# Performance work log

Hardware: AMD Instinct MI355X
Metric: run time of the kernel (lower is better)

The kernel has to match this reference:

```python
import jax, jax.numpy as jnp
import numpy as np

# Level-7 icosphere: nv vertices, nf faces
NV, NF = 163842, 327680
IN_C, NECK_C, OUT_C, B = 64, 32, 128, 2
EPS = 1e-5


def setup_inputs() -> dict:
    key = jax.random.key(0)
    ks = jax.random.split(key, 16)
    f32 = jnp.float32
    d = {}
    d['x'] = jax.random.normal(ks[0], (B, IN_C, NV), f32)
    # conv1 (1x1), bn1
    d['w1'] = jax.random.normal(ks[1], (NECK_C, IN_C), f32) * 0.05
    d['b1'] = jnp.zeros((NECK_C,), f32)
    d['gamma1'] = jnp.ones((NECK_C,), f32); d['beta1'] = jnp.zeros((NECK_C,), f32)
    # MeshConv: coeffs (out,in,4 taps: id, lap, grad_ew, grad_ns) + bias
    d['coeffs'] = jax.random.normal(ks[2], (NECK_C, NECK_C, 4), f32) * 0.05
    d['mc_bias'] = jnp.zeros((NECK_C,), f32)
    d['gamma2'] = jnp.ones((NECK_C,), f32); d['beta2'] = jnp.zeros((NECK_C,), f32)
    # conv3 (1x1), bn3
    d['w3'] = jax.random.normal(ks[3], (OUT_C, NECK_C), f32) * 0.05
    d['b3'] = jnp.zeros((OUT_C,), f32)
    d['gamma3'] = jnp.ones((OUT_C,), f32); d['beta3'] = jnp.zeros((OUT_C,), f32)
    # shortcut conv_ + bn_ (diff_chan since in!=out)
    d['wsc'] = jax.random.normal(ks[4], (OUT_C, IN_C), f32) * 0.05
    d['bsc'] = jnp.zeros((OUT_C,), f32)
    d['gammasc'] = jnp.ones((OUT_C,), f32); d['betasc'] = jnp.zeros((OUT_C,), f32)
    # sparse mesh operators (gather indices + values):
    # G: face gradient, 3 components per face from 3 face vertices
    d['idx_G'] = jax.random.randint(ks[5], (NF, 3), 0, NV, jnp.int32)
    d['vals_G'] = jax.random.normal(ks[6], (NF, 3, 3), f32) * 0.1
    # EW/NS tangent direction per face (3-vectors)
    d['EW'] = jax.random.normal(ks[7], (NF, 3), f32)
    d['NS'] = jax.random.normal(ks[8], (NF, 3), f32)
    # L: vertex laplacian, ~7 nnz per row
    d['idx_L'] = jax.random.randint(ks[9], (NV, 7), 0, NV, jnp.int32)
    d['vals_L'] = jax.random.normal(ks[10], (NV, 7), f32) * 0.1
    # F2V: face-to-vertex averaging, ~6 faces per vertex
    d['idx_F2V'] = jax.random.randint(ks[11], (NV, 6), 0, NF, jnp.int32)
    d['vals_F2V'] = jax.random.uniform(ks[12], (NV, 6), f32) / 6.0
    return d


def _bn(x, g, b):
    # training-mode BatchNorm1d over (batch, spatial), per channel
    m = x.mean(axis=(0, 2), keepdims=True)
    v = ((x - m) ** 2).mean(axis=(0, 2), keepdims=True)
    return g[None, :, None] * (x - m) * jax.lax.rsqrt(v + EPS) + b[None, :, None]


def _conv1x1(x, w, b):
    return jnp.einsum('oc,bcn->bon', w, x) + b[None, :, None]


def _mesh_conv(x, coeffs, bias, idx_G, vals_G, EW, NS, idx_L, vals_L, idx_F2V, vals_F2V):
    # laplacian: sparse matmul via gather  (B,C,NV)
    lap = jnp.einsum('bcnk,nk->bcn', x[:, :, idx_L], vals_L)
    # face gradient: (B,C,NF,3 components)
    grad_face = jnp.einsum('bcfj,fij->bcfi', x[:, :, idx_G], vals_G)
    g_ew = jnp.einsum('bcfi,fi->bcf', grad_face, EW)
    g_ns = jnp.einsum('bcfi,fi->bcf', grad_face, NS)
    # face -> vertex averaging
    gv_ew = jnp.einsum('bcnk,nk->bcn', g_ew[:, :, idx_F2V], vals_F2V)
    gv_ns = jnp.einsum('bcnk,nk->bcn', g_ns[:, :, idx_F2V], vals_F2V)
    feat = jnp.stack([x, lap, gv_ew, gv_ns], axis=-1)  # (B,C,NV,4)
    return jnp.einsum('bcnk,ock->bon', feat, coeffs) + bias[None, :, None]


def reference(x, w1, b1, gamma1, beta1, coeffs, mc_bias, gamma2, beta2,
              w3, b3, gamma3, beta3, wsc, bsc, gammasc, betasc,
              idx_G, vals_G, EW, NS, idx_L, vals_L, idx_F2V, vals_F2V):
    # shortcut branch (diff_chan)
    x2 = _bn(_conv1x1(x, wsc, bsc), gammasc, betasc)
    # main branch
    h = jax.nn.relu(_bn(_conv1x1(x, w1, b1), gamma1, beta1))
    h = _mesh_conv(h, coeffs, mc_bias, idx_G, vals_G, EW, NS, idx_L, vals_L, idx_F2V, vals_F2V)
    h = jax.nn.relu(_bn(h, gamma2, beta2))
    h = _bn(_conv1x1(h, w3, b3), gamma3, beta3)
    return jax.nn.relu(h + x2)
```

## Files before the change

kernel.cpp:

```cpp
#include <hip/hip_runtime.h>

#define NV   163842
#define NF   327680
#define BB   2
#define INC  64
#define NECK 32
#define OUTC 128
#define NT   (BB*NV)
#define EPSB 1e-5f

typedef unsigned short ushort_t;
typedef __attribute__((ext_vector_type(8))) short bf16x8;
typedef __attribute__((ext_vector_type(4))) float f32x4;

#define F_SX8  0
#define F_SS8  512
#define F_A1   33280
#define F_C1   33312
#define F_ASC  33344
#define F_CSC  33472
#define F_S2S  33600
#define F_S2Q  33632
#define F_A2   33664
#define F_C2   33696
#define F_SHR  33728
#define F_SS2  33760
#define F_A3   34784
#define F_C3   34912
#define F_CF   35040
#define STATN  35168
#define F_W1B  35200
#define F_CFB  36224
#define F_Y1   38272
#define F_H2   (F_Y1 + NT*16)
#define F_I18  (F_H2 + NT*16)
#define F_WEW  (F_I18 + NV*18)
#define F_WNS  (F_WEW + NV*18)
#define F_XB   (F_WNS + NV*18)

#define FSTR 136

__device__ __forceinline__ float bf2f(ushort_t u) {
    union { unsigned int i; float f; } x; x.i = ((unsigned int)u) << 16; return x.f;
}
__device__ __forceinline__ ushort_t f2bf(float f) {
    union { float f; unsigned int i; } x; x.f = f;
    unsigned int r = x.i + 0x7fffu + ((x.i >> 16) & 1u);
    return (ushort_t)(r >> 16);
}

__global__ __launch_bounds__(256) void k_xcvt(const float* __restrict__ x,
                                              float* __restrict__ ws,
                                              ushort_t* __restrict__ xb) {
    __shared__ float SSl[64 * 68 + 64];
    const int tid = threadIdx.x;
    const int w = tid >> 6, l = tid & 63;
    const int o16 = l & 15, kg = l >> 4;

    for (int i = tid; i < 64 * 68 + 64; i += 256) SSl[i] = 0.f;
    __syncthreads();

    f32x4 acc[10];
#pragma unroll
    for (int i = 0; i < 10; ++i) acc[i] = (f32x4){0.f, 0.f, 0.f, 0.f};
    f32x4 accS[4];
#pragma unroll
    for (int i = 0; i < 4; ++i) accS[i] = (f32x4){0.f, 0.f, 0.f, 0.f};

    bf16x8 onesf;
    {
        short ov = (o16 == 0) ? (short)0x3F80 : (short)0;
#pragma unroll
        for (int j = 0; j < 8; ++j) onesf[j] = ov;
    }

    const int NCHB = (NV + 63) >> 6;
    const int NW = gridDim.x * 4;
    for (int cid = blockIdx.x * 4 + w; cid < 2 * NCHB; cid += NW) {
        const int b = (cid >= NCHB) ? 1 : 0;
        const int tc = cid - b * NCHB;
        const int n0 = tc << 6;
        const float* xsrc = x + (size_t)b * 64 * NV;
        const bool full = (n0 + 64 <= NV);
        const int n = n0 + l;
        if (n < NV) {
            unsigned int pk[32];
#pragma unroll
            for (int c2 = 0; c2 < 32; ++c2) {
                float f0 = xsrc[(size_t)(2 * c2) * NV + n];
                float f1 = xsrc[(size_t)(2 * c2 + 1) * NV + n];
                pk[c2] = (unsigned int)f2bf(f0) | ((unsigned int)f2bf(f1) << 16);
            }
            ushort_t* row = xb + (size_t)(b * NV + n) * 64;
#pragma unroll
            for (int j = 0; j < 8; ++j) {
                uint4 q = make_uint4(pk[4 * j], pk[4 * j + 1], pk[4 * j + 2], pk[4 * j + 3]);
                *(uint4*)(row + j * 8) = q;
            }
        }
        bf16x8 fr[4][2];
#pragma unroll
        for (int mt = 0; mt < 4; ++mt) {
            const float* rp = xsrc + (size_t)(mt * 16 + o16) * NV + n0;
#pragma unroll
            for (int ks = 0; ks < 2; ++ks) {
                const int v0 = ks * 32 + kg * 8;
                float f[8];
                if (full) {
                    float4 q0 = *(const float4*)(rp + v0);
                    float4 q1 = *(const float4*)(rp + v0 + 4);
                    f[0] = q0.x; f[1] = q0.y; f[2] = q0.z; f[3] = q0.w;
                    f[4] = q1.x; f[5] = q1.y; f[6] = q1.z; f[7] = q1.w;
                } else {
#pragma unroll
                    for (int j = 0; j < 8; ++j)
                        f[j] = (n0 + v0 + j < NV) ? rp[v0 + j] : 0.f;
                }
                bf16x8 fb;
#pragma unroll
                for (int j = 0; j < 8; ++j) fb[j] = (short)f2bf(f[j]);
                fr[mt][ks] = fb;
            }
        }
#pragma unroll
        for (int ks = 0; ks < 2; ++ks) {
            int tt = 0;
#pragma unroll
            for (int mt = 0; mt < 4; ++mt) {
#pragma unroll
                for (int nt2 = 0; nt2 < 4; ++nt2) {
                    if (nt2 >= mt) {
                        acc[tt] = __builtin_amdgcn_mfma_f32_16x16x32_bf16(fr[mt][ks], fr[nt2][ks], acc[tt], 0, 0, 0);
                        ++tt;
                    }
                }
                accS[mt] = __builtin_amdgcn_mfma_f32_16x16x32_bf16(onesf, fr[mt][ks], accS[mt], 0, 0, 0);
            }
        }
    }
    {
        int tt = 0;
#pragma unroll
        for (int mt = 0; mt < 4; ++mt) {
#pragma unroll
            for (int nt2 = 0; nt2 < 4; ++nt2) {
                if (nt2 >= mt) {
#pragma unroll
                    for (int r = 0; r < 4; ++r) {
                        const int row = mt * 16 + kg * 4 + r;
                        const int col = nt2 * 16 + o16;
                        atomicAdd(&SSl[row * 68 + col], acc[tt][r]);
                    }
                    ++tt;
                }
            }
            if (kg == 0) atomicAdd(&SSl[64 * 68 + mt * 16 + o16], accS[mt][0]);
        }
    }
    __syncthreads();
    {
        float* SSg = ws + F_SS8 + (size_t)(blockIdx.x & 7) * 4096;
        for (int i = tid; i < 64 * 64; i += 256) {
            const int r = i >> 6, c = i & 63;
            if (c >= r) {
                float v = SSl[r * 68 + c];
                if (v != 0.f) atomicAdd(&SSg[r * 64 + c], v);
            }
        }
        if (tid < 64) atomicAdd(&ws[F_SX8 + (blockIdx.x & 7) * 64 + tid], SSl[64 * 68 + tid]);
    }
}

__global__ __launch_bounds__(256) void k_fold1(const float* __restrict__ w1,
                                               const float* __restrict__ g1,
                                               const float* __restrict__ be1,
                                               const float* __restrict__ wsc,
                                               const float* __restrict__ gsc,
                                               const float* __restrict__ besc,
                                               float* __restrict__ ws,
                                               ushort_t* __restrict__ w1b) {
    __shared__ float SSl[4096];
    __shared__ float Sxl[64];
    const int tid = threadIdx.x;
    for (int i = tid; i < 4096; i += 256) {
        const int r = i >> 6, c = i & 63;
        float v = 0.f;
        if (c >= r) {
#pragma unroll
            for (int s = 0; s < 8; ++s) v += ws[F_SS8 + s * 4096 + i];
        }
        SSl[i] = v;
    }
    if (tid < 64) {
        float v = 0.f;
#pragma unroll
        for (int s = 0; s < 8; ++s) v += ws[F_SX8 + s * 64 + tid];
        Sxl[tid] = v;
    }
    __syncthreads();
    for (int i = tid; i < 4096; i += 256) {
        const int r = i >> 6, c = i & 63;
        if (c < r) SSl[i] = SSl[c * 64 + r];
    }
    __syncthreads();
    if (tid >= 32) return;
    const int bk = blockIdx.x;
    const float* w;
    float gamma, beta;
    float *pa, *pc;
    if (bk == 0) {
        w = w1 + tid * 64; gamma = g1[tid]; beta = be1[tid];
        pa = ws + F_A1 + tid; pc = ws + F_C1 + tid;
    } else {
        int o = (bk - 1) * 32 + tid;
        w = wsc + o * 64; gamma = gsc[o]; beta = besc[o];
        pa = ws + F_ASC + o; pc = ws + F_CSC + o;
    }
    float4 wr[16];
#pragma unroll
    for (int i = 0; i < 16; ++i) wr[i] = *(const float4*)(w + i * 4);
    float dotm = 0.f, quad = 0.f;
#pragma unroll
    for (int i4 = 0; i4 < 16; ++i4) {
        float4 wi = wr[i4];
        float rd[4] = {0.f, 0.f, 0.f, 0.f};
#pragma unroll
        for (int j4 = 0; j4 < 16; ++j4) {
            float4 wj = wr[j4];
#pragma unroll
            for (int r = 0; r < 4; ++r) {
                const float* row = &SSl[(i4 * 4 + r) * 64 + j4 * 4];
                rd[r] += row[0] * wj.x + row[1] * wj.y + row[2] * wj.z + row[3] * wj.w;
            }
        }
        dotm += wi.x * Sxl[i4 * 4] + wi.y * Sxl[i4 * 4 + 1] + wi.z * Sxl[i4 * 4 + 2] + wi.w * Sxl[i4 * 4 + 3];
        quad += wi.x * rd[0] + wi.y * rd[1] + wi.z * rd[2] + wi.w * rd[3];
    }
    const float invN = 1.0f / (float)NT;
    const float mean0 = dotm * invN;
    const float var = quad * invN - mean0 * mean0;
    const float a = gamma * rsqrtf(var + EPSB);
    *pa = a;
    *pc = beta - a * mean0;
    if (bk == 0) {
#pragma unroll
        for (int i4 = 0; i4 < 16; ++i4) {
            w1b[tid * 64 + i4 * 4 + 0] = f2bf(a * wr[i4].x);
            w1b[tid * 64 + i4 * 4 + 1] = f2bf(a * wr[i4].y);
            w1b[tid * 64 + i4 * 4 + 2] = f2bf(a * wr[i4].z);
            w1b[tid * 64 + i4 * 4 + 3] = f2bf(a * wr[i4].w);
        }
    }
}

__global__ __launch_bounds__(256) void k_conv1(const ushort_t* __restrict__ xb,
                                               const ushort_t* __restrict__ w1b,
                                               const float* __restrict__ ws,
                                               ushort_t* __restrict__ y1) {
    const int tid = threadIdx.x;
    const int w = tid >> 6, l = tid & 63;
    const int o16 = l & 15, kg = l >> 4;
    bf16x8 af[2][2];
#pragma unroll
    for (int mt = 0; mt < 2; ++mt)
#pragma unroll
        for (int ks = 0; ks < 2; ++ks)
            af[mt][ks] = *(const bf16x8*)(w1b + (mt * 16 + o16) * 64 + ks * 32 + kg * 8);
    float c1r[2][4];
#pragma unroll
    for (int mt = 0; mt < 2; ++mt)
#pragma unroll
        for (int r = 0; r < 4; ++r)
            c1r[mt][r] = ws[F_C1 + mt * 16 + kg * 4 + r];

    const int NCH = (NT + 63) >> 6;
    for (int ch = blockIdx.x * 4 + w; ch < NCH; ch += gridDim.x * 4) {
        const int n0 = ch << 6;
        bf16x8 bf[4][2];
#pragma unroll
        for (int nt = 0; nt < 4; ++nt) {
            int row = n0 + nt * 16 + o16;
            row = row < NT ? row : NT - 1;
#pragma unroll
            for (int ks = 0; ks < 2; ++ks)
                bf[nt][ks] = *(const bf16x8*)(xb + (size_t)row * 64 + ks * 32 + kg * 8);
        }
        f32x4 acc[2][4];
#pragma unroll
        for (int mt = 0; mt < 2; ++mt)
#pragma unroll
            for (int nt = 0; nt < 4; ++nt) acc[mt][nt] = (f32x4){0.f, 0.f, 0.f, 0.f};
#pragma unroll
        for (int mt = 0; mt < 2; ++mt)
#pragma unroll
            for (int nt = 0; nt < 4; ++nt)
#pragma unroll
                for (int ks = 0; ks < 2; ++ks)
                    acc[mt][nt] = __builtin_amdgcn_mfma_f32_16x16x32_bf16(af[mt][ks], bf[nt][ks], acc[mt][nt], 0, 0, 0);
#pragma unroll
        for (int nt = 0; nt < 4; ++nt) {
            const int vert = n0 + nt * 16 + o16;
            if (vert < NT) {
#pragma unroll
                for (int mt = 0; mt < 2; ++mt) {
                    uint2 p;
                    p.x = (unsigned)f2bf(fmaxf(acc[mt][nt][0] + c1r[mt][0], 0.f)) |
                          ((unsigned)f2bf(fmaxf(acc[mt][nt][1] + c1r[mt][1], 0.f)) << 16);
                    p.y = (unsigned)f2bf(fmaxf(acc[mt][nt][2] + c1r[mt][2], 0.f)) |
                          ((unsigned)f2bf(fmaxf(acc[mt][nt][3] + c1r[mt][3], 0.f)) << 16);
                    *(uint2*)(y1 + (size_t)vert * 32 + mt * 16 + kg * 4) = p;
                }
            }
        }
    }
}

__global__ __launch_bounds__(256) void k_w18(const int* __restrict__ idx_F2V,
                                             const float* __restrict__ vals_F2V,
                                             const int* __restrict__ idx_G,
                                             const float* __restrict__ vals_G,
                                             const float* __restrict__ EW,
                                             const float* __restrict__ NS,
                                             int* __restrict__ i18,
                                             float* __restrict__ wew,
                                             float* __restrict__ wns) {
    const int n = blockIdx.x * 256 + threadIdx.x;
    if (n >= NV) return;
#pragma unroll
    for (int k = 0; k < 6; ++k) {
        int f = idx_F2V[n * 6 + k];
        float fv = vals_F2V[n * 6 + k];
        float e0 = EW[f * 3], e1 = EW[f * 3 + 1], e2 = EW[f * 3 + 2];
        float s0 = NS[f * 3], s1 = NS[f * 3 + 1], s2 = NS[f * 3 + 2];
#pragma unroll
        for (int j = 0; j < 3; ++j) {
            float g0 = vals_G[f * 9 + j], g1 = vals_G[f * 9 + 3 + j], g2 = vals_G[f * 9 + 6 + j];
            i18[n * 18 + k * 3 + j] = idx_G[f * 3 + j];
            wew[n * 18 + k * 3 + j] = fv * (g0 * e0 + g1 * e1 + g2 * e2);
            wns[n * 18 + k * 3 + j] = fv * (g0 * s0 + g1 * s1 + g2 * s2);
        }
    }
}

__global__ __launch_bounds__(256) void k_cvtcoef(const float* __restrict__ c,
                                                 ushort_t* __restrict__ cb) {
    int i = blockIdx.x * 256 + threadIdx.x;
    if (i < 4096) cb[i] = f2bf(c[i]);
}

__global__ __launch_bounds__(256, 4) void k_meshconv(const ushort_t* __restrict__ y1,
                                                     const ushort_t* __restrict__ cfb,
                                                     const int* __restrict__ idx_L,
                                                     const float* __restrict__ vals_L,
                                                     const int* __restrict__ i18,
                                                     const float* __restrict__ w18ew,
                                                     const float* __restrict__ w18ns,
                                                     ushort_t* __restrict__ h2,
                                                     float* __restrict__ ws) {
    __shared__ __align__(16) ushort_t feat[4][32 * FSTR];
    __shared__ float sred[64];
    const int tid = threadIdx.x;
    const int w = __builtin_amdgcn_readfirstlane(tid >> 6);
    const int lane = tid & 63;
    ushort_t* fw = &feat[w][0];
    const int gh = lane >> 5;
    const int bh = (lane >> 4) & 1;
    const int c2 = lane & 15;
    const int ybase = bh * (NV * 32);
    const int o16 = lane & 15;
    const int kg = lane >> 4;

    if (tid < 64) sred[tid] = 0.f;
    __syncthreads();

    float ssum[8], sssq[8];
#pragma unroll
    for (int i = 0; i < 8; ++i) { ssum[i] = 0.f; sssq[i] = 0.f; }

    const int gw = blockIdx.x * 4 + w;
    const int NW = gridDim.x * 4;
    const int NCH = (NV + 15) >> 4;

    for (int ch = gw; ch < NCH; ch += NW) {
        const int n0 = ch << 4;
        for (int jj = 0; jj < 8; ++jj) {
            const int gA = 2 * jj;
            const int nA = n0 + gA;
            const int nB = nA + 1;
            const int nnA = (nA < NV) ? nA : NV - 1;
            const int nnB = (nB < NV) ? nB : NV - 1;
            const int n = n0 + gA + gh;
            const bool ok = (n < NV);
            const int nn = gh ? nnB : nnA;
            const ushort_t* yb = y1 + ybase;
            unsigned int qs = *(const unsigned int*)(yb + (nn << 5) + (c2 << 1));
            float fx0 = bf2f((ushort_t)(qs & 0xffffu));
            float fx1 = bf2f((ushort_t)(qs >> 16));
            float lap0 = 0.f, lap1 = 0.f, ge0 = 0.f, ge1 = 0.f, gn0 = 0.f, gn1 = 0.f;
#pragma unroll
            for (int j = 0; j < 7; ++j) {
                const int viA = idx_L[nnA * 7 + j];
                const int viB = idx_L[nnB * 7 + j];
                const float wvA = vals_L[nnA * 7 + j];
                const float wvB = vals_L[nnB * 7 + j];
                const int vi = gh ? viB : viA;
                const float wv = gh ? wvB : wvA;
                unsigned int q = *(const unsigned int*)(yb + (vi << 5) + (c2 << 1));
                lap0 += wv * bf2f((ushort_t)(q & 0xffffu));
                lap1 += wv * bf2f((ushort_t)(q >> 16));
            }
#pragma unroll
            for (int j = 0; j < 18; ++j) {
                const int viA = i18[nnA * 18 + j];
                const int viB = i18[nnB * 18 + j];
                const float weA = w18ew[nnA * 18 + j];
                const float weB = w18ew[nnB * 18 + j];
                const float wnA = w18ns[nnA * 18 + j];
                const float wnB = w18ns[nnB * 18 + j];
                const int vi = gh ? viB : viA;
                const float we = gh ? weB : weA;
                const float wn = gh ? wnB : wnA;
                unsigned int q = *(const unsigned int*)(yb + (vi << 5) + (c2 << 1));
                float v0 = bf2f((ushort_t)(q & 0xffffu));
                float v1 = bf2f((ushort_t)(q >> 16));
                ge0 += we * v0; ge1 += we * v1;
                gn0 += wn * v0; gn1 += wn * v1;
            }
            unsigned int u0 = 0u, u1 = 0u, u2 = 0u, u3 = 0u;
            if (ok) {
                u0 = (unsigned int)f2bf(fx0) | ((unsigned int)f2bf(lap0) << 16);
                u1 = (unsigned int)f2bf(ge0) | ((unsigned int)f2bf(gn0) << 16);
                u2 = (unsigned int)f2bf(fx1) | ((unsigned int)f2bf(lap1) << 16);
                u3 = (unsigned int)f2bf(ge1) | ((unsigned int)f2bf(gn1) << 16);
            }
            const int inst = bh * 16 + gA + gh;
            *(uint4*)(fw + inst * FSTR + (c2 << 3)) = make_uint4(u0, u1, u2, u3);
        }
        f32x4 acc[2][2];
#pragma unroll
        for (int mt = 0; mt < 2; ++mt)
#pragma unroll
            for (int nt = 0; nt < 2; ++nt) acc[mt][nt] = (f32x4){0.f, 0.f, 0.f, 0.f};
        bf16x8 bfr[2][4];
#pragma unroll
        for (int nt = 0; nt < 2; ++nt)
#pragma unroll
            for (int kt = 0; kt < 4; ++kt)
                bfr[nt][kt] = *(const bf16x8*)(fw + (nt * 16 + o16) * FSTR + kt * 32 + kg * 8);
#pragma unroll
        for (int mt = 0; mt < 2; ++mt) {
#pragma unroll
            for (int kt = 0; kt < 4; ++kt) {
                bf16x8 af = *(const bf16x8*)(cfb + (mt * 16 + o16) * 128 + kt * 32 + kg * 8);
                acc[mt][0] = __builtin_amdgcn_mfma_f32_16x16x32_bf16(af, bfr[0][kt], acc[mt][0], 0, 0, 0);
                acc[mt][1] = __builtin_amdgcn_mfma_f32_16x16x32_bf16(af, bfr[1][kt], acc[mt][1], 0, 0, 0);
            }
        }
        const int n = n0 + o16;
        if (n < NV) {
#pragma unroll
            for (int nt = 0; nt < 2; ++nt) {
                const int rowb = ((nt * NV + n) << 5);
#pragma unroll
                for (int mt = 0; mt < 2; ++mt) {
#pragma unroll
                    for (int r = 0; r < 4; ++r) {
                        float v = acc[mt][nt][r];
                        int o = mt * 16 + kg * 4 + r;
                        h2[rowb + o] = f2bf(v);
                        ssum[mt * 4 + r] += v;
                        sssq[mt * 4 + r] += v * v;
                    }
                }
            }
        }
    }

#pragma unroll
    for (int si = 0; si < 8; ++si) {
#pragma unroll
        for (int m = 1; m < 16; m <<= 1) {
            ssum[si] += __shfl_xor(ssum[si], m, 16);
            sssq[si] += __shfl_xor(sssq[si], m, 16);
        }
    }
    if (o16 == 0) {
#pragma unroll
        for (int mt = 0; mt < 2; ++mt)
#pragma unroll
            for (int r = 0; r < 4; ++r) {
                int o = mt * 16 + kg * 4 + r;
                atomicAdd(&sred[o], ssum[mt * 4 + r]);
                atomicAdd(&sred[32 + o], sssq[mt * 4 + r]);
            }
    }
    __syncthreads();
    if (tid < 64) atomicAdd(&ws[F_S2S + tid], sred[tid]);
}

__global__ void k_fold2(const float* __restrict__ g2, const float* __restrict__ be2,
                        float* __restrict__ ws) {
    const int c = threadIdx.x;
    if (c < 32) {
        const float invN = 1.0f / (float)NT;
        float m = ws[F_S2S + c] * invN;
        float var = ws[F_S2Q + c] * invN - m * m;
        float a = g2[c] * rsqrtf(var + EPSB);
        ws[F_A2 + c] = a;
        ws[F_C2 + c] = be2[c] - a * m;
    }
}

__global__ __launch_bounds__(256) void k_hrmoments(const ushort_t* __restrict__ h2,
                                                   float* __restrict__ ws) {
    __shared__ __align__(16) ushort_t tile[4][32 * 40];
    __shared__ float red[1056];
    const int tid = threadIdx.x;
    const int w = tid >> 6, l = tid & 63;
    ushort_t* T = &tile[w][0];
    const int c8 = (l & 3) * 8;
    const int v0 = l >> 2;
    const int fr = l & 15, kg = l >> 4;

    for (int i = tid; i < 1056; i += 256) red[i] = 0.f;
    __syncthreads();

    float a2r[8], c2r[8];
#pragma unroll
    for (int j = 0; j < 8; ++j) { a2r[j] = ws[F_A2 + c8 + j]; c2r[j] = ws[F_C2 + c8 + j]; }

    f32x4 acc[2][2];
#pragma unroll
    for (int a = 0; a < 2; ++a)
#pragma unroll
        for (int b = 0; b < 2; ++b) acc[a][b] = (f32x4){0.f, 0.f, 0.f, 0.f};
    float ssum[8];
#pragma unroll
    for (int j = 0; j < 8; ++j) ssum[j] = 0.f;

    const int NCH = (NT + 31) >> 5;
    for (int ch = blockIdx.x * 4 + w; ch < NCH; ch += gridDim.x * 4) {
        const int s0 = ch << 5;
#pragma unroll
        for (int i = 0; i < 2; ++i) {
            const int vert = i * 16 + v0;
            const int s = s0 + vert;
            uint4 q = make_uint4(0u, 0u, 0u, 0u);
            const bool ok = (s < NT);
            if (ok) q = *(const uint4*)(h2 + (size_t)s * 32 + c8);
            const ushort_t* qs = (const ushort_t*)&q;
            ushort_t hb[8];
#pragma unroll
            for (int j = 0; j < 8; ++j) {
                float hv = ok ? fmaxf(a2r[j] * bf2f(qs[j]) + c2r[j], 0.f) : 0.f;
                ssum[j] += hv;
                hb[j] = f2bf(hv);
            }
#pragma unroll
            for (int j = 0; j < 8; ++j) T[(c8 + j) * 40 + vert] = hb[j];
        }
        bf16x8 f0 = *(const bf16x8*)(T + fr * 40 + kg * 8);
        bf16x8 f1 = *(const bf16x8*)(T + (16 + fr) * 40 + kg * 8);
        acc[0][0] = __builtin_amdgcn_mfma_f32_16x16x32_bf16(f0, f0, acc[0][0], 0, 0, 0);
        acc[0][1] = __builtin_amdgcn_mfma_f32_16x16x32_bf16(f0, f1, acc[0][1], 0, 0, 0);
        acc[1][0] = __builtin_amdgcn_mfma_f32_16x16x32_bf16(f1, f0, acc[1][0], 0, 0, 0);
        acc[1][1] = __builtin_amdgcn_mfma_f32_16x16x32_bf16(f1, f1, acc[1][1], 0, 0, 0);
    }
#pragma unroll
    for (int mt = 0; mt < 2; ++mt)
#pragma unroll
        for (int nt = 0; nt < 2; ++nt)
#pragma unroll
            for (int r = 0; r < 4; ++r)
                atomicAdd(&red[(mt * 16 + kg * 4 + r) * 32 + nt * 16 + fr], acc[mt][nt][r]);
#pragma unroll
    for (int j = 0; j < 8; ++j) {
        float s = ssum[j];
        s += __shfl_xor(s, 4); s += __shfl_xor(s, 8);
        s += __shfl_xor(s, 16); s += __shfl_xor(s, 32);
        if (v0 == 0) atomicAdd(&red[1024 + c8 + j], s);
    }
    __syncthreads();
    for (int i = tid; i < 1024; i += 256) atomicAdd(&ws[F_SS2 + i], red[i]);
    if (tid < 32) atomicAdd(&ws[F_SHR + tid], red[1024 + tid]);
}

__global__ __launch_bounds__(128) void k_fold3(const float* __restrict__ w3,
                                               const float* __restrict__ wsc,
                                               const float* __restrict__ g3,
                                               const float* __restrict__ be3,
                                               float* __restrict__ ws,
                                               ushort_t* __restrict__ wfb) {
    __shared__ float SSl[1024];
    __shared__ float Sl[32];
    const int tid = threadIdx.x;
    for (int i = tid; i < 1024; i += 128) SSl[i] = ws[F_SS2 + i];
    if (tid < 32) Sl[tid] = ws[F_SHR + tid];
    __syncthreads();
    const int o = tid;
    float4 wr[8];
#pragma unroll
    for (int i = 0; i < 8; ++i) wr[i] = *(const float4*)(w3 + o * 32 + i * 4);
    float dotm = 0.f, quad = 0.f;
#pragma unroll
    for (int i4 = 0; i4 < 8; ++i4) {
        float4 wi = wr[i4];
        float rd[4] = {0.f, 0.f, 0.f, 0.f};
#pragma unroll
        for (int j4 = 0; j4 < 8; ++j4) {
            float4 wj = wr[j4];
#pragma unroll
            for (int r = 0; r < 4; ++r) {
                const float* row = &SSl[(i4 * 4 + r) * 32 + j4 * 4];
                rd[r] += row[0] * wj.x + row[1] * wj.y + row[2] * wj.z + row[3] * wj.w;
            }
        }
        dotm += wi.x * Sl[i4 * 4] + wi.y * Sl[i4 * 4 + 1] + wi.z * Sl[i4 * 4 + 2] + wi.w * Sl[i4 * 4 + 3];
        quad += wi.x * rd[0] + wi.y * rd[1] + wi.z * rd[2] + wi.w * rd[3];
    }
    const float invN = 1.0f / (float)NT;
    const float mean0 = dotm * invN;
    const float var = quad * invN - mean0 * mean0;
    const float a = g3[o] * rsqrtf(var + EPSB);
    const float cbias = be3[o] - a * mean0;
    ws[F_A3 + o] = a;
    ws[F_C3 + o] = cbias;
    const float asc = ws[F_ASC + o], csc = ws[F_CSC + o];
    ws[F_CF + o] = cbias + csc;
#pragma unroll
    for (int i4 = 0; i4 < 8; ++i4) {
        wfb[o * 96 + i4 * 4 + 0] = f2bf(a * wr[i4].x);
        wfb[o * 96 + i4 * 4 + 1] = f2bf(a * wr[i4].y);
        wfb[o * 96 + i4 * 4 + 2] = f2bf(a * wr[i4].z);
        wfb[o * 96 + i4 * 4 + 3] = f2bf(a * wr[i4].w);
    }
    for (int j = 0; j < 64; ++j)
        wfb[o * 96 + 32 + j] = f2bf(asc * wsc[o * 64 + j]);
}

__global__ __launch_bounds__(256) void k_final(const ushort_t* __restrict__ xb,
                                               const ushort_t* __restrict__ h2,
                                               const ushort_t* __restrict__ wfb,
                                               const float* __restrict__ ws,
                                               float* __restrict__ out) {
    __shared__ __align__(16) ushort_t feat[32 * 104];
    __shared__ __align__(16) float ol[128][33];
    const int tid = threadIdx.x;
    const int w = tid >> 6, l = tid & 63;
    const int fr = l & 15, kg = l >> 4;

    bf16x8 af[2][3];
#pragma unroll
    for (int mt = 0; mt < 2; ++mt)
#pragma unroll
        for (int kt = 0; kt < 3; ++kt)
            af[mt][kt] = *(const bf16x8*)(wfb + (w * 32 + mt * 16 + fr) * 96 + kt * 32 + kg * 8);
    float cfr[2][4];
#pragma unroll
    for (int mt = 0; mt < 2; ++mt)
#pragma unroll
        for (int r = 0; r < 4; ++r)
            cfr[mt][r] = ws[F_CF + w * 32 + mt * 16 + kg * 4 + r];

    const int hv = tid >> 3, hc4 = (tid & 7) * 4;
    float a2r[4], c2r[4];
#pragma unroll
    for (int j = 0; j < 4; ++j) { a2r[j] = ws[F_A2 + hc4 + j]; c2r[j] = ws[F_C2 + hc4 + j]; }
    const int xv = tid >> 3, xseg = tid & 7;
    const int oo = tid >> 1, ohalf = tid & 1;

    const int NCHK = (NV + 31) >> 5;
    for (int cid = blockIdx.x; cid < 2 * NCHK; cid += gridDim.x) {
        const int b = (cid >= NCHK) ? 1 : 0;
        const int t = cid - b * NCHK;
        const int n0 = t << 5;
        const int rem = NV - n0 < 32 ? NV - n0 : 32;
        {
            const int s = b * NV + n0 + hv;
            const bool ok = (hv < rem);
            uint2 q = make_uint2(0u, 0u);
            if (ok) q = *(const uint2*)(h2 + (size_t)s * 32 + hc4);
            const ushort_t* qs = (const ushort_t*)&q;
            unsigned int p0 = 0u, p1 = 0u;
            if (ok) {
                float h0 = fmaxf(a2r[0] * bf2f(qs[0]) + c2r[0], 0.f);
                float h1 = fmaxf(a2r[1] * bf2f(qs[1]) + c2r[1], 0.f);
                float h2v = fmaxf(a2r[2] * bf2f(qs[2]) + c2r[2], 0.f);
                float h3 = fmaxf(a2r[3] * bf2f(qs[3]) + c2r[3], 0.f);
                p0 = (unsigned int)f2bf(h0) | ((unsigned int)f2bf(h1) << 16);
                p1 = (unsigned int)f2bf(h2v) | ((unsigned int)f2bf(h3) << 16);
            }
            *(uint2*)(feat + hv * 104 + hc4) = make_uint2(p0, p1);
        }
        {
            const int s = b * NV + n0 + xv;
            uint4 q = make_uint4(0u, 0u, 0u, 0u);
            if (xv < rem) q = *(const uint4*)(xb + (size_t)s * 64 + xseg * 8);
            *(uint4*)(feat + xv * 104 + 32 + xseg * 8) = q;
        }
        __syncthreads();
        bf16x8 bf[2][3];
#pragma unroll
        for (int nt = 0; nt < 2; ++nt)
#pragma unroll
            for (int kt = 0; kt < 3; ++kt)
                bf[nt][kt] = *(const bf16x8*)(feat + (nt * 16 + fr) * 104 + kt * 32 + kg * 8);
        f32x4 acc[2][2];
#pragma unroll
        for (int mt = 0; mt < 2; ++mt)
#pragma unroll
            for (int nt = 0; nt < 2; ++nt) acc[mt][nt] = (f32x4){0.f, 0.f, 0.f, 0.f};
#pragma unroll
        for (int mt = 0; mt < 2; ++mt)
#pragma unroll
            for (int nt = 0; nt < 2; ++nt)
#pragma unroll
                for (int kt = 0; kt < 3; ++kt)
                    acc[mt][nt] = __builtin_amdgcn_mfma_f32_16x16x32_bf16(af[mt][kt], bf[nt][kt], acc[mt][nt], 0, 0, 0);
#pragma unroll
        for (int mt = 0; mt < 2; ++mt)
#pragma unroll
            for (int nt = 0; nt < 2; ++nt)
#pragma unroll
                for (int r = 0; r < 4; ++r)
                    ol[w * 32 + mt * 16 + kg * 4 + r][nt * 16 + fr] =
                        fmaxf(acc[mt][nt][r] + cfr[mt][r], 0.f);
        __syncthreads();
        {
            float* po = out + (size_t)(b * 128 + oo) * NV + n0 + ohalf * 16;
            if (rem == 32) {
#pragma unroll
                for (int j2 = 0; j2 < 8; ++j2)
                    *(float2*)(po + j2 * 2) = make_float2(ol[oo][ohalf * 16 + j2 * 2],
                                                         ol[oo][ohalf * 16 + j2 * 2 + 1]);
            } else {
#pragma unroll
                for (int j = 0; j < 16; ++j) {
                    int v = ohalf * 16 + j;
                    if (v < rem) po[j] = ol[oo][v];
                }
            }
        }
        __syncthreads();
    }
}

extern "C" void kernel_launch(void* const* d_in, const int* in_sizes, int n_in,
                              void* d_out, int out_size, void* d_ws, size_t ws_size,
                              hipStream_t stream) {
    (void)in_sizes; (void)n_in; (void)out_size; (void)ws_size;
    const float* x        = (const float*)d_in[0];
    const float* w1       = (const float*)d_in[1];
    const float* g1       = (const float*)d_in[3];
    const float* be1      = (const float*)d_in[4];
    const float* coeffs   = (const float*)d_in[5];
    const float* g2       = (const float*)d_in[7];
    const float* be2      = (const float*)d_in[8];
    const float* w3       = (const float*)d_in[9];
    const float* g3       = (const float*)d_in[11];
    const float* be3      = (const float*)d_in[12];
    const float* wsc      = (const float*)d_in[13];
    const float* gsc      = (const float*)d_in[15];
    const float* besc     = (const float*)d_in[16];
    const int*   idx_G    = (const int*)d_in[17];
    const float* vals_G   = (const float*)d_in[18];
    const float* EW       = (const float*)d_in[19];
    const float* NS       = (const float*)d_in[20];
    const int*   idx_L    = (const int*)d_in[21];
    const float* vals_L   = (const float*)d_in[22];
    const int*   idx_F2V  = (const int*)d_in[23];
    const float* vals_F2V = (const float*)d_in[24];
    float* ws  = (float*)d_ws;
    float* out = (float*)d_out;

    ushort_t* w1b = (ushort_t*)(ws + F_W1B);
    ushort_t* cfb = (ushort_t*)(ws + F_CFB);
    ushort_t* y1  = (ushort_t*)(ws + F_Y1);
    ushort_t* h2  = (ushort_t*)(ws + F_H2);
    ushort_t* xb  = (ushort_t*)(ws + F_XB);
    ushort_t* wfb = (ushort_t*)(ws + F_Y1);

    hipMemsetAsync(ws, 0, STATN * sizeof(float), stream);
    hipLaunchKernelGGL(k_xcvt, dim3(1280), dim3(256), 0, stream, x, ws, xb);
    hipLaunchKernelGGL(k_w18, dim3((NV + 255) / 256), dim3(256), 0, stream,
                       idx_F2V, vals_F2V, idx_G, vals_G, EW, NS,
                       (int*)(ws + F_I18), ws + F_WEW, ws + F_WNS);
    hipLaunchKernelGGL(k_cvtcoef, dim3(16), dim3(256), 0, stream, coeffs, cfb);
    hipLaunchKernelGGL(k_fold1, dim3(5), dim3(256), 0, stream, w1, g1, be1, wsc, gsc, besc, ws, w1b);
    hipLaunchKernelGGL(k_conv1, dim3(1280), dim3(256), 0, stream, xb, w1b, ws, y1);
    hipLaunchKernelGGL(k_meshconv, dim3(1024), dim3(256), 0, stream,
                       y1, cfb, idx_L, vals_L,
                       (const int*)(ws + F_I18), ws + F_WEW, ws + F_WNS,
                       h2, ws);
    hipLaunchKernelGGL(k_fold2, dim3(1), dim3(32), 0, stream, g2, be2, ws);
    hipLaunchKernelGGL(k_hrmoments, dim3(1024), dim3(256), 0, stream, h2, ws);
    hipLaunchKernelGGL(k_fold3, dim3(1), dim3(128), 0, stream, w3, wsc, g3, be3, ws, wfb);
    hipLaunchKernelGGL(k_final, dim3(2048), dim3(256), 0, stream, xb, h2, wfb, ws, out);
}
```

Before: 542.6 us.

## Remap meshconv lanes to four vertices per batch and store final output directly

The meshconv kernel now gives each wave 32 vertices of a single batch, with four vertices per instruction group instead of two vertices across both batches. This drops the duplicated index and weight loads plus the selects that picked between the two candidates. In the final kernel the LDS transpose buffer and its extra barrier are removed, and each lane writes its MFMA results straight to global memory with 16-lane contiguous stores. That trades the fully coalesced float2 row writes for narrower direct stores but cuts LDS traffic and one sync per chunk.

```diff
diff --git a/kernel.cpp b/kernel.cpp
--- a/kernel.cpp
+++ b/kernel.cpp
@@ -363,10 +363,8 @@
     const int w = __builtin_amdgcn_readfirstlane(tid >> 6);
     const int lane = tid & 63;
     ushort_t* fw = &feat[w][0];
-    const int gh = lane >> 5;
-    const int bh = (lane >> 4) & 1;
+    const int v4 = lane >> 4;
     const int c2 = lane & 15;
-    const int ybase = bh * (NV * 32);
     const int o16 = lane & 15;
     const int kg = lane >> 4;
 
@@ -379,47 +377,38 @@
 
     const int gw = blockIdx.x * 4 + w;
     const int NW = gridDim.x * 4;
-    const int NCH = (NV + 15) >> 4;
-
-    for (int ch = gw; ch < NCH; ch += NW) {
-        const int n0 = ch << 4;
+    const int NCHB = (NV + 31) >> 5;
+
+    for (int cid = gw; cid < 2 * NCHB; cid += NW) {
+        const int b = (cid >= NCHB) ? 1 : 0;
+        const int vch = cid - b * NCHB;
+        const int n0 = vch << 5;
+        const ushort_t* yb = y1 + (size_t)b * (NV * 32);
         for (int jj = 0; jj < 8; ++jj) {
-            const int gA = 2 * jj;
-            const int nA = n0 + gA;
-            const int nB = nA + 1;
-            const int nnA = (nA < NV) ? nA : NV - 1;
-            const int nnB = (nB < NV) ? nB : NV - 1;
-            const int n = n0 + gA + gh;
+            const int n = n0 + jj * 4 + v4;
             const bool ok = (n < NV);
-            const int nn = gh ? nnB : nnA;
-            const ushort_t* yb = y1 + ybase;
+            const int nn = ok ? n : NV - 1;
             unsigned int qs = *(const unsigned int*)(yb + (nn << 5) + (c2 << 1));
             float fx0 = bf2f((ushort_t)(qs & 0xffffu));
             float fx1 = bf2f((ushort_t)(qs >> 16));
             float lap0 = 0.f, lap1 = 0.f, ge0 = 0.f, ge1 = 0.f, gn0 = 0.f, gn1 = 0.f;
+            const int* ilp = idx_L + nn * 7;
+            const float* vlp = vals_L + nn * 7;
 #pragma unroll
             for (int j = 0; j < 7; ++j) {
-                const int viA = idx_L[nnA * 7 + j];
-                const int viB = idx_L[nnB * 7 + j];
-                const float wvA = vals_L[nnA * 7 + j];
-                const float wvB = vals_L[nnB * 7 + j];
-                const int vi = gh ? viB : viA;
-                const float wv = gh ? wvB : wvA;
+                const int vi = ilp[j];
+                const float wv = vlp[j];
                 unsigned int q = *(const unsigned int*)(yb + (vi << 5) + (c2 << 1));
                 lap0 += wv * bf2f((ushort_t)(q & 0xffffu));
                 lap1 += wv * bf2f((ushort_t)(q >> 16));
             }
+            const int* igp = i18 + nn * 18;
+            const float* wep = w18ew + nn * 18;
+            const float* wnp = w18ns + nn * 18;
 #pragma unroll
             for (int j = 0; j < 18; ++j) {
-                const int viA = i18[nnA * 18 + j];
-                const int viB = i18[nnB * 18 + j];
-                const float weA = w18ew[nnA * 18 + j];
-                const float weB = w18ew[nnB * 18 + j];
-                const float wnA = w18ns[nnA * 18 + j];
-                const float wnB = w18ns[nnB * 18 + j];
-                const int vi = gh ? viB : viA;
-                const float we = gh ? weB : weA;
-                const float wn = gh ? wnB : wnA;
+                const int vi = igp[j];
+                const float we = wep[j], wn = wnp[j];
                 unsigned int q = *(const unsigned int*)(yb + (vi << 5) + (c2 << 1));
                 float v0 = bf2f((ushort_t)(q & 0xffffu));
                 float v1 = bf2f((ushort_t)(q >> 16));
@@ -433,7 +422,7 @@
                 u2 = (unsigned int)f2bf(fx1) | ((unsigned int)f2bf(lap1) << 16);
                 u3 = (unsigned int)f2bf(ge1) | ((unsigned int)f2bf(gn1) << 16);
             }
-            const int inst = bh * 16 + gA + gh;
+            const int inst = jj * 4 + v4;
             *(uint4*)(fw + inst * FSTR + (c2 << 3)) = make_uint4(u0, u1, u2, u3);
         }
         f32x4 acc[2][2];
@@ -456,11 +445,11 @@
                 acc[mt][1] = __builtin_amdgcn_mfma_f32_16x16x32_bf16(af, bfr[1][kt], acc[mt][1], 0, 0, 0);
             }
         }
-        const int n = n0 + o16;
-        if (n < NV) {
-#pragma unroll
-            for (int nt = 0; nt < 2; ++nt) {
-                const int rowb = ((nt * NV + n) << 5);
+#pragma unroll
+        for (int nt = 0; nt < 2; ++nt) {
+            const int vert = n0 + nt * 16 + o16;
+            if (vert < NV) {
+                const int rowb = ((b * NV + vert) << 5);
 #pragma unroll
                 for (int mt = 0; mt < 2; ++mt) {
 #pragma unroll
@@ -644,7 +633,6 @@
                                                const float* __restrict__ ws,
                                                float* __restrict__ out) {
     __shared__ __align__(16) ushort_t feat[32 * 104];
-    __shared__ __align__(16) float ol[128][33];
     const int tid = threadIdx.x;
     const int w = tid >> 6, l = tid & 63;
     const int fr = l & 15, kg = l >> 4;
@@ -667,7 +655,6 @@
 #pragma unroll
     for (int j = 0; j < 4; ++j) { a2r[j] = ws[F_A2 + hc4 + j]; c2r[j] = ws[F_C2 + hc4 + j]; }
     const int xv = tid >> 3, xseg = tid & 7;
-    const int oo = tid >> 1, ohalf = tid & 1;
 
     const int NCHK = (NV + 31) >> 5;
     for (int cid = blockIdx.x; cid < 2 * NCHK; cid += gridDim.x) {
@@ -705,6 +692,7 @@
 #pragma unroll
             for (int kt = 0; kt < 3; ++kt)
                 bf[nt][kt] = *(const bf16x8*)(feat + (nt * 16 + fr) * 104 + kt * 32 + kg * 8);
+        __syncthreads();
         f32x4 acc[2][2];
 #pragma unroll
         for (int mt = 0; mt < 2; ++mt)
@@ -718,30 +706,18 @@
                 for (int kt = 0; kt < 3; ++kt)
                     acc[mt][nt] = __builtin_amdgcn_mfma_f32_16x16x32_bf16(af[mt][kt], bf[nt][kt], acc[mt][nt], 0, 0, 0);
 #pragma unroll
-        for (int mt = 0; mt < 2; ++mt)
-#pragma unroll
-            for (int nt = 0; nt < 2; ++nt)
-#pragma unroll
-                for (int r = 0; r < 4; ++r)
-                    ol[w * 32 + mt * 16 + kg * 4 + r][nt * 16 + fr] =
-                        fmaxf(acc[mt][nt][r] + cfr[mt][r], 0.f);
-        __syncthreads();
-        {
-            float* po = out + (size_t)(b * 128 + oo) * NV + n0 + ohalf * 16;
-            if (rem == 32) {
-#pragma unroll
-                for (int j2 = 0; j2 < 8; ++j2)
-                    *(float2*)(po + j2 * 2) = make_float2(ol[oo][ohalf * 16 + j2 * 2],
-                                                         ol[oo][ohalf * 16 + j2 * 2 + 1]);
-            } else {
-#pragma unroll
-                for (int j = 0; j < 16; ++j) {
-                    int v = ohalf * 16 + j;
-                    if (v < rem) po[j] = ol[oo][v];
+        for (int mt = 0; mt < 2; ++mt) {
+#pragma unroll
+            for (int nt = 0; nt < 2; ++nt) {
+                const int col = n0 + nt * 16 + fr;
+                if (col < NV) {
+                    float* po = out + (size_t)(b * 128 + w * 32 + mt * 16 + kg * 4) * NV + col;
+#pragma unroll
+                    for (int r = 0; r < 4; ++r)
+                        po[(size_t)r * NV] = fmaxf(acc[mt][nt][r] + cfr[mt][r], 0.f);
                 }
             }
         }
-        __syncthreads();
     }
 }
 
```

After: 544.3 us. No clear change (+0.3%).

## Merge prep kernels, fold BN2 finalize into moments, store final output directly

Applied to the files above, without the earlier changes.

Three changes:
- The per-vertex gradient-weight precompute and the coefficient bf16 conversion are merged into one kernel.
- The single-block BN2 fold kernel is removed; each k_hrmoments block now computes the BN2 scale and shift itself into shared memory and also writes them to the workspace.
- In the final kernel, the LDS staging tile and its two per-chunk barriers are dropped; ReLU'd MFMA accumulators are stored straight to global memory in 16-float row segments.
The aim is to cut two launches and the LDS round-trip, at the risk of less coalesced output writes on the largest store stream.

```diff
diff --git a/kernel.cpp b/kernel.cpp
--- a/kernel.cpp
+++ b/kernel.cpp
@@ -49,6 +49,37 @@
     return (ushort_t)(r >> 16);
 }
 
+__global__ __launch_bounds__(256) void k_prep(const int* __restrict__ idx_F2V,
+                                              const float* __restrict__ vals_F2V,
+                                              const int* __restrict__ idx_G,
+                                              const float* __restrict__ vals_G,
+                                              const float* __restrict__ EW,
+                                              const float* __restrict__ NS,
+                                              const float* __restrict__ coeffs,
+                                              int* __restrict__ i18,
+                                              float* __restrict__ wew,
+                                              float* __restrict__ wns,
+                                              ushort_t* __restrict__ cfb) {
+    const int gid = blockIdx.x * 256 + threadIdx.x;
+    if (gid < 4096) cfb[gid] = f2bf(coeffs[gid]);
+    const int n = gid;
+    if (n >= NV) return;
+#pragma unroll
+    for (int k = 0; k < 6; ++k) {
+        int f = idx_F2V[n * 6 + k];
+        float fv = vals_F2V[n * 6 + k];
+        float e0 = EW[f * 3], e1 = EW[f * 3 + 1], e2 = EW[f * 3 + 2];
+        float s0 = NS[f * 3], s1 = NS[f * 3 + 1], s2 = NS[f * 3 + 2];
+#pragma unroll
+        for (int j = 0; j < 3; ++j) {
+            float g0 = vals_G[f * 9 + j], g1 = vals_G[f * 9 + 3 + j], g2 = vals_G[f * 9 + 6 + j];
+            i18[n * 18 + k * 3 + j] = idx_G[f * 3 + j];
+            wew[n * 18 + k * 3 + j] = fv * (g0 * e0 + g1 * e1 + g2 * e2);
+            wns[n * 18 + k * 3 + j] = fv * (g0 * s0 + g1 * s1 + g2 * s2);
+        }
+    }
+}
+
 __global__ __launch_bounds__(256) void k_xcvt(const float* __restrict__ x,
                                               float* __restrict__ ws,
                                               ushort_t* __restrict__ xb) {
@@ -313,39 +344,6 @@
             }
         }
     }
-}
-
-__global__ __launch_bounds__(256) void k_w18(const int* __restrict__ idx_F2V,
-                                             const float* __restrict__ vals_F2V,
-                                             const int* __restrict__ idx_G,
-                                             const float* __restrict__ vals_G,
-                                             const float* __restrict__ EW,
-                                             const float* __restrict__ NS,
-                                             int* __restrict__ i18,
-                                             float* __restrict__ wew,
-                                             float* __restrict__ wns) {
-    const int n = blockIdx.x * 256 + threadIdx.x;
-    if (n >= NV) return;
-#pragma unroll
-    for (int k = 0; k < 6; ++k) {
-        int f = idx_F2V[n * 6 + k];
-        float fv = vals_F2V[n * 6 + k];
-        float e0 = EW[f * 3], e1 = EW[f * 3 + 1], e2 = EW[f * 3 + 2];
-        float s0 = NS[f * 3], s1 = NS[f * 3 + 1], s2 = NS[f * 3 + 2];
-#pragma unroll
-        for (int j = 0; j < 3; ++j) {
-            float g0 = vals_G[f * 9 + j], g1 = vals_G[f * 9 + 3 + j], g2 = vals_G[f * 9 + 6 + j];
-            i18[n * 18 + k * 3 + j] = idx_G[f * 3 + j];
-            wew[n * 18 + k * 3 + j] = fv * (g0 * e0 + g1 * e1 + g2 * e2);
-            wns[n * 18 + k * 3 + j] = fv * (g0 * s0 + g1 * s1 + g2 * s2);
-        }
-    }
-}
-
-__global__ __launch_bounds__(256) void k_cvtcoef(const float* __restrict__ c,
-                                                 ushort_t* __restrict__ cb) {
-    int i = blockIdx.x * 256 + threadIdx.x;
-    if (i < 4096) cb[i] = f2bf(c[i]);
 }
 
 __global__ __launch_bounds__(256, 4) void k_meshconv(const ushort_t* __restrict__ y1,
@@ -498,23 +496,13 @@
     if (tid < 64) atomicAdd(&ws[F_S2S + tid], sred[tid]);
 }
 
-__global__ void k_fold2(const float* __restrict__ g2, const float* __restrict__ be2,
-                        float* __restrict__ ws) {
-    const int c = threadIdx.x;
-    if (c < 32) {
-        const float invN = 1.0f / (float)NT;
-        float m = ws[F_S2S + c] * invN;
-        float var = ws[F_S2Q + c] * invN - m * m;
-        float a = g2[c] * rsqrtf(var + EPSB);
-        ws[F_A2 + c] = a;
-        ws[F_C2 + c] = be2[c] - a * m;
-    }
-}
-
 __global__ __launch_bounds__(256) void k_hrmoments(const ushort_t* __restrict__ h2,
+                                                   const float* __restrict__ g2,
+                                                   const float* __restrict__ be2,
                                                    float* __restrict__ ws) {
     __shared__ __align__(16) ushort_t tile[4][32 * 40];
     __shared__ float red[1056];
+    __shared__ float sA2[32], sC2[32];
     const int tid = threadIdx.x;
     const int w = tid >> 6, l = tid & 63;
     ushort_t* T = &tile[w][0];
@@ -522,12 +510,21 @@
     const int v0 = l >> 2;
     const int fr = l & 15, kg = l >> 4;
 
+    if (tid < 32) {
+        const float invN = 1.0f / (float)NT;
+        float m = ws[F_S2S + tid] * invN;
+        float var = ws[F_S2Q + tid] * invN - m * m;
+        float a = g2[tid] * rsqrtf(var + EPSB);
+        float c = be2[tid] - a * m;
+        sA2[tid] = a; sC2[tid] = c;
+        ws[F_A2 + tid] = a; ws[F_C2 + tid] = c;
+    }
     for (int i = tid; i < 1056; i += 256) red[i] = 0.f;
     __syncthreads();
 
     float a2r[8], c2r[8];
 #pragma unroll
-    for (int j = 0; j < 8; ++j) { a2r[j] = ws[F_A2 + c8 + j]; c2r[j] = ws[F_C2 + c8 + j]; }
+    for (int j = 0; j < 8; ++j) { a2r[j] = sA2[c8 + j]; c2r[j] = sC2[c8 + j]; }
 
     f32x4 acc[2][2];
 #pragma unroll
@@ -644,7 +641,6 @@
                                                const float* __restrict__ ws,
                                                float* __restrict__ out) {
     __shared__ __align__(16) ushort_t feat[32 * 104];
-    __shared__ __align__(16) float ol[128][33];
     const int tid = threadIdx.x;
     const int w = tid >> 6, l = tid & 63;
     const int fr = l & 15, kg = l >> 4;
@@ -667,7 +663,6 @@
 #pragma unroll
     for (int j = 0; j < 4; ++j) { a2r[j] = ws[F_A2 + hc4 + j]; c2r[j] = ws[F_C2 + hc4 + j]; }
     const int xv = tid >> 3, xseg = tid & 7;
-    const int oo = tid >> 1, ohalf = tid & 1;
 
     const int NCHK = (NV + 31) >> 5;
     for (int cid = blockIdx.x; cid < 2 * NCHK; cid += gridDim.x) {
@@ -705,6 +700,7 @@
 #pragma unroll
             for (int kt = 0; kt < 3; ++kt)
                 bf[nt][kt] = *(const bf16x8*)(feat + (nt * 16 + fr) * 104 + kt * 32 + kg * 8);
+        __syncthreads();
         f32x4 acc[2][2];
 #pragma unroll
         for (int mt = 0; mt < 2; ++mt)
@@ -718,30 +714,18 @@
                 for (int kt = 0; kt < 3; ++kt)
                     acc[mt][nt] = __builtin_amdgcn_mfma_f32_16x16x32_bf16(af[mt][kt], bf[nt][kt], acc[mt][nt], 0, 0, 0);
 #pragma unroll
-        for (int mt = 0; mt < 2; ++mt)
-#pragma unroll
-            for (int nt = 0; nt < 2; ++nt)
-#pragma unroll
-                for (int r = 0; r < 4; ++r)
-                    ol[w * 32 + mt * 16 + kg * 4 + r][nt * 16 + fr] =
-                        fmaxf(acc[mt][nt][r] + cfr[mt][r], 0.f);
-        __syncthreads();
-        {
-            float* po = out + (size_t)(b * 128 + oo) * NV + n0 + ohalf * 16;
-            if (rem == 32) {
-#pragma unroll
-                for (int j2 = 0; j2 < 8; ++j2)
-                    *(float2*)(po + j2 * 2) = make_float2(ol[oo][ohalf * 16 + j2 * 2],
-                                                         ol[oo][ohalf * 16 + j2 * 2 + 1]);
-            } else {
-#pragma unroll
-                for (int j = 0; j < 16; ++j) {
-                    int v = ohalf * 16 + j;
-                    if (v < rem) po[j] = ol[oo][v];
+        for (int mt = 0; mt < 2; ++mt) {
+#pragma unroll
+            for (int nt = 0; nt < 2; ++nt) {
+                const int col = n0 + nt * 16 + fr;
+                if (col < NV) {
+                    float* po = out + (size_t)(b * 128 + w * 32 + mt * 16 + kg * 4) * NV + col;
+#pragma unroll
+                    for (int r = 0; r < 4; ++r)
+                        po[(size_t)r * NV] = fmaxf(acc[mt][nt][r] + cfr[mt][r], 0.f);
                 }
             }
         }
-        __syncthreads();
     }
 }
 
@@ -781,19 +765,17 @@
     ushort_t* wfb = (ushort_t*)(ws + F_Y1);
 
     hipMemsetAsync(ws, 0, STATN * sizeof(float), stream);
+    hipLaunchKernelGGL(k_prep, dim3((NV + 255) / 256), dim3(256), 0, stream,
+                       idx_F2V, vals_F2V, idx_G, vals_G, EW, NS, coeffs,
+                       (int*)(ws + F_I18), ws + F_WEW, ws + F_WNS, cfb);
     hipLaunchKernelGGL(k_xcvt, dim3(1280), dim3(256), 0, stream, x, ws, xb);
-    hipLaunchKernelGGL(k_w18, dim3((NV + 255) / 256), dim3(256), 0, stream,
-                       idx_F2V, vals_F2V, idx_G, vals_G, EW, NS,
-                       (int*)(ws + F_I18), ws + F_WEW, ws + F_WNS);
-    hipLaunchKernelGGL(k_cvtcoef, dim3(16), dim3(256), 0, stream, coeffs, cfb);
     hipLaunchKernelGGL(k_fold1, dim3(5), dim3(256), 0, stream, w1, g1, be1, wsc, gsc, besc, ws, w1b);
     hipLaunchKernelGGL(k_conv1, dim3(1280), dim3(256), 0, stream, xb, w1b, ws, y1);
     hipLaunchKernelGGL(k_meshconv, dim3(1024), dim3(256), 0, stream,
                        y1, cfb, idx_L, vals_L,
                        (const int*)(ws + F_I18), ws + F_WEW, ws + F_WNS,
                        h2, ws);
-    hipLaunchKernelGGL(k_fold2, dim3(1), dim3(32), 0, stream, g2, be2, ws);
-    hipLaunchKernelGGL(k_hrmoments, dim3(1024), dim3(256), 0, stream, h2, ws);
+    hipLaunchKernelGGL(k_hrmoments, dim3(1024), dim3(256), 0, stream, h2, g2, be2, ws);
     hipLaunchKernelGGL(k_fold3, dim3(1), dim3(128), 0, stream, w3, wsc, g3, be3, ws, wfb);
     hipLaunchKernelGGL(k_final, dim3(2048), dim3(256), 0, stream, xb, h2, wfb, ws, out);
 }
```

Result: no change. 538.3 us (-0.8%).
